# Kernel optimization log

Hardware: AMD Instinct MI355X
Metric: run time of the kernel (lower is better)

Reference implementation:

```python
import jax, jax.numpy as jnp
import numpy as np

B, N, DIM, H, DH, K = 4, 2048, 512, 6, 64, 16
KEEP_PROB = 0.9  # 1 - dropout_rate
LOG2PI = float(np.log(2.0 * np.pi))
LOG_PRIOR = float(np.log(1.0 / K))


def setup_inputs() -> dict:
    key = jax.random.key(0)
    ks = jax.random.split(key, 7)
    inputs_q = jax.random.normal(ks[0], (B, N, DIM), dtype=jnp.float32)
    # decoder-style causal mask, shape [B, 1, q_len, kv_len]
    causal = jnp.tril(jnp.ones((N, N), dtype=jnp.float32))
    mask = jnp.broadcast_to(causal[None, None], (B, 1, N, N))
    # dropout keep mask broadcast across the query dim: [B, H, 1, kv_len]
    keep = jax.random.bernoulli(ks[1], KEEP_PROB, (B, H, 1, N)).astype(jnp.float32)
    w_qkv = jax.random.normal(ks[2], (DIM, 3 * H * DH), dtype=jnp.float32) * 0.02
    w_out = jax.random.normal(ks[3], (H * DH, DIM), dtype=jnp.float32) * 0.02
    mu_lookup = jax.random.normal(ks[4], (K, DIM), dtype=jnp.float32)
    logvar_lookup = jax.random.normal(ks[5], (K, DIM), dtype=jnp.float32) * 0.1
    return {
        "inputs_q": inputs_q,
        "mask": mask,
        "keep": keep,
        "w_qkv": w_qkv,
        "w_out": w_out,
        "mu_lookup": mu_lookup,
        "logvar_lookup": logvar_lookup,
    }


def reference(inputs_q, mask, keep, w_qkv, w_out, mu_lookup, logvar_lookup):
    # --- MultiHeadDotProductAttention (self-attn path) ---
    qkv = (inputs_q @ w_qkv).reshape(B, N, 3, H, DH)  # [B,N,3,H,DH]
    q, k, v = qkv[:, :, 0], qkv[:, :, 1], qkv[:, :, 2]
    # bias: 0 where mask > 0, -1e10 elsewhere (note: no 1/sqrt(d) scaling, as in source)
    bias = jnp.where(mask > 0, 0.0, -1e10)
    attn_weights = jnp.einsum('bqhd,bkhd->bhqk', q, k) + bias  # [B,H,N,N]
    attn_weights = jax.nn.softmax(attn_weights, axis=-1)
    # broadcast dropout: mask shared across the query dim
    attn_weights = attn_weights * keep / KEEP_PROB
    attn_out = jnp.einsum('bhqk,bkhd->bqhd', attn_weights, v)
    attn_out = attn_out.reshape(B, N, H * DH) @ w_out  # [B,N,DIM]

    # --- GMM posterior approx q(y|x) ~= p(y|z) (approx_qy_x, vectorized over k) ---
    z = attn_out.mean(axis=1)  # pooled latent, [B,DIM]
    diff = z[:, None, :] - mu_lookup[None]  # [B,K,DIM]
    llh = -0.5 * jnp.sum(
        diff * diff / jnp.exp(logvar_lookup)[None] + logvar_lookup[None] + LOG2PI,
        axis=-1,
    )  # [B,K]
    logLogit_qy_x = llh + LOG_PRIOR
    qy_x = jax.nn.softmax(logLogit_qy_x, axis=1)  # [B,K]

    # combine mixture mean back in so both branches are live in one output
    return attn_out + (qy_x @ mu_lookup)[:, None, :]
```

## Files before the change

kernel.cpp:

```cpp
#include <hip/hip_runtime.h>
#include <cstdint>
#include <cstddef>

#define NH 6
#define NSEQ 2048
#define DIMD 512
#define BATCH 4
#define HD 384
#define LOG2PI_F 1.8378770664093453f

typedef __attribute__((ext_vector_type(8))) short short8;
typedef __attribute__((ext_vector_type(8))) unsigned short ushort8;
typedef __attribute__((ext_vector_type(4))) unsigned short ushort4v;
typedef __attribute__((ext_vector_type(4))) float floatx4;

__device__ inline unsigned short f2bf(float f){
  unsigned int u = __float_as_uint(f);
  u += 0x7FFFu + ((u>>16)&1u);
  return (unsigned short)(u>>16);
}

#define GLD16(gp, lp) __builtin_amdgcn_global_load_lds( \
  (const __attribute__((address_space(1))) void*)(gp), \
  (__attribute__((address_space(3))) void*)(lp), 16, 0, 0)

__global__ __launch_bounds__(256) void convert_x(
    const float* __restrict__ xq, unsigned short* __restrict__ xbf)
{
  int i = blockIdx.x*256 + threadIdx.x;
  floatx4 v = *(const floatx4*)(xq + (size_t)i*4);
  ushort4v r;
  #pragma unroll
  for(int j=0;j<4;j++) r[j] = f2bf(v[j]);
  *(ushort4v*)(xbf + (size_t)i*4) = r;
}

__global__ __launch_bounds__(256) void wtrans(
    const float* __restrict__ src, unsigned short* __restrict__ dst, int R, int C)
{
  __shared__ __attribute__((aligned(16))) unsigned short Ls[64*72];
  const int t = threadIdx.x;
  const int r = t>>2, c0 = (t&3)*16;
  const int d0 = blockIdx.y*64, n0 = blockIdx.x*64;
  #pragma unroll
  for (int j=0;j<16;j+=4){
    floatx4 v = *(const floatx4*)(src + (size_t)(d0+r)*C + n0 + c0 + j);
    #pragma unroll
    for(int jj=0;jj<4;jj++) Ls[r*72 + c0+j+jj] = f2bf(v[jj]);
  }
  __syncthreads();
  #pragma unroll
  for (int j=0;j<16;j+=8){
    ushort8 o;
    #pragma unroll
    for(int jj=0;jj<8;jj++) o[jj] = Ls[(c0+j+jj)*72 + r];
    *(ushort8*)(dst + (size_t)(n0+r)*R + d0 + c0 + j) = o;
  }
}

__global__ __launch_bounds__(256) void gemm_qkv(
    const unsigned short* __restrict__ A,
    const unsigned short* __restrict__ Bt,
    const float* __restrict__ keep,
    unsigned short* __restrict__ Qo, unsigned short* __restrict__ Ko, unsigned short* __restrict__ Vt)
{
  __shared__ __attribute__((aligned(16))) unsigned short As[128*64];
  __shared__ __attribute__((aligned(16))) unsigned short Bs[128*64];
  const int tid = threadIdx.x;
  const int w = tid>>6, lane = tid&63;
  const int wr = w>>1, wc = w&1;
  const int quad = lane>>4, l16 = lane&15;
  const int tM = blockIdx.y*128, tN = blockIdx.x*128;
  const int r8 = lane>>3, c8 = (lane&7)*8;
  floatx4 acc[4][4];
  floatx4 zed = {0.f,0.f,0.f,0.f};
  #pragma unroll
  for (int i=0;i<4;i++)
    #pragma unroll
    for(int j=0;j<4;j++) acc[i][j] = zed;

  for (int k0=0; k0<512; k0+=64){
    #pragma unroll
    for (int i=0;i<4;i++){
      int row = w*32 + i*8;
      GLD16(A  + (size_t)(tM+row+r8)*512 + k0 + c8, As + row*64);
      GLD16(Bt + (size_t)(tN+row+r8)*512 + k0 + c8, Bs + row*64);
    }
    __syncthreads();
    #pragma unroll
    for (int kk=0; kk<64; kk+=32){
      short8 af[4], bf[4];
      #pragma unroll
      for(int mt=0;mt<4;mt++)
        af[mt] = *(const short8*)(As + (wr*64+mt*16+l16)*64 + kk + quad*8);
      #pragma unroll
      for(int nt=0;nt<4;nt++)
        bf[nt] = *(const short8*)(Bs + (wc*64+nt*16+l16)*64 + kk + quad*8);
      #pragma unroll
      for(int mt=0;mt<4;mt++)
        #pragma unroll
        for(int nt=0;nt<4;nt++)
          acc[mt][nt] = __builtin_amdgcn_mfma_f32_16x16x32_bf16(af[mt], bf[nt], acc[mt][nt], 0,0,0);
    }
    __syncthreads();
  }
  #pragma unroll
  for(int nt=0;nt<4;nt++){
    int gcol = tN + wc*64 + nt*16 + l16;
    int t = gcol/384;
    int rem = gcol - t*384;
    int h = rem>>6, dh = rem&63;
    #pragma unroll
    for(int mt=0;mt<4;mt++){
      int grow = tM + wr*64 + mt*16 + quad*4;
      #pragma unroll
      for(int r=0;r<4;r++){
        int row = grow + r;
        int b = row>>11, n = row & 2047;
        if (t==0)      Qo[(size_t)((b*NH + h)*NSEQ + n)*64 + dh] = f2bf(acc[mt][nt][r]);
        else if (t==1) Ko[(size_t)((b*NH + h)*NSEQ + n)*64 + dh] = f2bf(acc[mt][nt][r]);
        else {
          float kp = keep[(size_t)(b*NH + h)*NSEQ + n];
          Vt[(size_t)((b*NH + h)*64 + dh)*NSEQ + n] = f2bf(acc[mt][nt][r]*kp);
        }
      }
    }
  }
}

__global__ __launch_bounds__(256,3) void attn_kernel(
    const unsigned short* __restrict__ Qg, const unsigned short* __restrict__ Kg,
    const unsigned short* __restrict__ VtG,
    unsigned short* __restrict__ atp)
{
  __shared__ __attribute__((aligned(16))) unsigned short Ks[64*64];
  __shared__ __attribute__((aligned(16))) unsigned short Vs[64*64];
  __shared__ __attribute__((aligned(16))) unsigned short Ps[4*32*72];
  const int tid = threadIdx.x;
  const int w = tid>>6, lane = tid&63;
  const int quad = lane>>4, l16 = lane&15;
  const int bx = 15 - (int)blockIdx.x;
  const int bh = blockIdx.y;
  const int b = bh/NH, h = bh - b*NH;
  const unsigned short* Qb = Qg  + (size_t)bh*NSEQ*64;
  const unsigned short* Kb = Kg  + (size_t)bh*NSEQ*64;
  const unsigned short* Vb = VtG + (size_t)bh*64*NSEQ;
  const int q0 = bx*128 + w*32;
  const int nkt_w  = 2*bx + 1 + (w>>1);
  const int nkt_max= 2*bx + 2;
  const int gr = lane>>3, gc = (lane&7)*8;

  short8 qf[2][2];
  #pragma unroll
  for(int mt=0;mt<2;mt++)
    #pragma unroll
    for(int kc=0;kc<2;kc++)
      qf[mt][kc] = *(const short8*)(Qb + (size_t)(q0+mt*16+l16)*64 + kc*32 + quad*8);

  short8 onesf;
  #pragma unroll
  for(int j=0;j<8;j++) onesf[j] = (short)0x3F80;

  floatx4 O[2][4];
  floatx4 accl[2];
  floatx4 zed = {0.f,0.f,0.f,0.f};
  #pragma unroll
  for(int mt=0;mt<2;mt++){
    #pragma unroll
    for(int dt=0;dt<4;dt++) O[mt][dt] = zed;
    accl[mt] = zed;
  }
  unsigned short* Pw = Ps + w*2304;

  for (int kt=0; kt<nkt_max; kt++){
    const int kB = kt*64;
    #pragma unroll
    for(int ro=0; ro<2; ro++){
      int r0 = ro*32 + w*8;
      GLD16(Kb + (size_t)(kB + r0 + gr)*64 + gc, Ks + r0*64);
      GLD16(Vb + (size_t)(r0 + gr)*NSEQ + kB + gc, Vs + r0*64);
    }
    __syncthreads();
    if (kt < nkt_w){
      short8 kf[4][2];
      #pragma unroll
      for(int nt=0;nt<4;nt++)
        #pragma unroll
        for(int kc=0;kc<2;kc++)
          kf[nt][kc] = *(const short8*)(Ks + (nt*16+l16)*64 + kc*32 + quad*8);

      floatx4 sacc[2][4];
      floatx4 m12 = {-12.f,-12.f,-12.f,-12.f};
      #pragma unroll
      for(int mt=0;mt<2;mt++)
        #pragma unroll
        for(int nt=0;nt<4;nt++) sacc[mt][nt] = m12;
      #pragma unroll
      for(int mt=0;mt<2;mt++)
        #pragma unroll
        for(int nt=0;nt<4;nt++)
          #pragma unroll
          for(int kc=0;kc<2;kc++)
            sacc[mt][nt] = __builtin_amdgcn_mfma_f32_16x16x32_bf16(qf[mt][kc], kf[nt][kc], sacc[mt][nt], 0,0,0);

      const bool dia = (kt == nkt_w-1);
      #pragma unroll
      for(int mt=0;mt<2;mt++){
        #pragma unroll
        for(int nt=0;nt<4;nt++){
          int key = kB + nt*16 + l16;
          #pragma unroll
          for(int r=0;r<4;r++){
            float p = __expf(sacc[mt][nt][r]);
            if (dia) p = (key <= q0 + mt*16 + quad*4 + r) ? p : 0.f;
            Pw[(mt*16+quad*4+r)*72 + nt*16 + l16] = f2bf(p);
          }
        }
      }
      short8 vf[2][4];
      #pragma unroll
      for(int kh=0;kh<2;kh++)
        #pragma unroll
        for(int dt=0;dt<4;dt++)
          vf[kh][dt] = *(const short8*)(Vs + (dt*16+l16)*64 + kh*32 + quad*8);
      #pragma unroll
      for(int kh=0;kh<2;kh++){
        #pragma unroll
        for(int mt=0;mt<2;mt++){
          short8 pf = *(const short8*)(Pw + (mt*16+l16)*72 + kh*32 + quad*8);
          accl[mt] = __builtin_amdgcn_mfma_f32_16x16x32_bf16(pf, onesf, accl[mt], 0,0,0);
          #pragma unroll
          for(int dt=0;dt<4;dt++)
            O[mt][dt] = __builtin_amdgcn_mfma_f32_16x16x32_bf16(pf, vf[kh][dt], O[mt][dt], 0,0,0);
        }
      }
    }
    __syncthreads();
  }

  #pragma unroll
  for(int mt=0;mt<2;mt++){
    #pragma unroll
    for(int r=0;r<4;r++){
      int q = q0 + mt*16 + quad*4 + r;
      float sc = (1.0f/0.9f) / accl[mt][r];
      #pragma unroll
      for(int dt=0;dt<4;dt++)
        atp[((size_t)(b*NSEQ + q))*HD + h*64 + dt*16 + l16] = f2bf(O[mt][dt][r]*sc);
    }
  }
}

__global__ __launch_bounds__(256) void gemm_proj(
    const unsigned short* __restrict__ A,
    const unsigned short* __restrict__ Bt,
    float* __restrict__ Co,
    float* __restrict__ z)
{
  __shared__ __attribute__((aligned(16))) unsigned short As[128*64];
  __shared__ __attribute__((aligned(16))) unsigned short Bs[128*64];
  const int tid = threadIdx.x;
  const int w = tid>>6, lane = tid&63;
  const int wr = w>>1, wc = w&1;
  const int quad = lane>>4, l16 = lane&15;
  const int tM = blockIdx.y*128, tN = blockIdx.x*128;
  const int r8 = lane>>3, c8 = (lane&7)*8;
  floatx4 acc[4][4];
  floatx4 zed = {0.f,0.f,0.f,0.f};
  #pragma unroll
  for (int i=0;i<4;i++)
    #pragma unroll
    for(int j=0;j<4;j++) acc[i][j] = zed;

  for (int k0=0; k0<384; k0+=64){
    #pragma unroll
    for (int i=0;i<4;i++){
      int row = w*32 + i*8;
      GLD16(A  + (size_t)(tM+row+r8)*384 + k0 + c8, As + row*64);
      GLD16(Bt + (size_t)(tN+row+r8)*384 + k0 + c8, Bs + row*64);
    }
    __syncthreads();
    #pragma unroll
    for (int kk=0; kk<64; kk+=32){
      short8 af[4], bf[4];
      #pragma unroll
      for(int mt=0;mt<4;mt++)
        af[mt] = *(const short8*)(As + (wr*64+mt*16+l16)*64 + kk + quad*8);
      #pragma unroll
      for(int nt=0;nt<4;nt++)
        bf[nt] = *(const short8*)(Bs + (wc*64+nt*16+l16)*64 + kk + quad*8);
      #pragma unroll
      for(int mt=0;mt<4;mt++)
        #pragma unroll
        for(int nt=0;nt<4;nt++)
          acc[mt][nt] = __builtin_amdgcn_mfma_f32_16x16x32_bf16(af[mt], bf[nt], acc[mt][nt], 0,0,0);
    }
    __syncthreads();
  }
  #pragma unroll
  for(int mt=0;mt<4;mt++){
    int grow = tM + wr*64 + mt*16 + quad*4;
    #pragma unroll
    for(int nt=0;nt<4;nt++){
      int gcol = tN + wc*64 + nt*16 + l16;
      #pragma unroll
      for(int r=0;r<4;r++)
        Co[(size_t)(grow+r)*512 + gcol] = acc[mt][nt][r];
    }
  }
  #pragma unroll
  for(int nt=0;nt<4;nt++){
    float s = 0.f;
    #pragma unroll
    for(int mt=0;mt<4;mt++)
      #pragma unroll
      for(int r=0;r<4;r++) s += acc[mt][nt][r];
    s += __shfl_xor(s, 16, 64);
    s += __shfl_xor(s, 32, 64);
    if (quad == 0){
      int gcol = tN + wc*64 + nt*16 + l16;
      atomicAdd(&z[(tM>>11)*DIMD + gcol], s);
    }
  }
}

__global__ __launch_bounds__(256) void gmm_kernel(
    const float* __restrict__ z, const float* __restrict__ mu,
    const float* __restrict__ lv, float* __restrict__ c)
{
  __shared__ float sh[16];
  __shared__ float qy[16];
  int tid = threadIdx.x;
  int k = tid>>4, li = tid&15;
  int b = blockIdx.x;
  float part = 0.f;
  for(int d=li; d<DIMD; d+=16){
    float zz = z[b*DIMD+d] * (1.0f/2048.0f);
    float m = mu[k*DIMD+d], l = lv[k*DIMD+d];
    float diff = zz - m;
    part += diff*diff*__expf(-l) + l + LOG2PI_F;
  }
  #pragma unroll
  for(int off=8;off>=1;off>>=1) part += __shfl_xor(part, off, 64);
  if (li==0) sh[k] = part;
  __syncthreads();
  if (tid<16){
    float logit = -0.5f*sh[tid];
    float mx = logit;
    #pragma unroll
    for(int off=8;off>=1;off>>=1) mx = fmaxf(mx, __shfl_xor(mx, off, 64));
    float e = __expf(logit-mx);
    float se = e;
    #pragma unroll
    for(int off=8;off>=1;off>>=1) se += __shfl_xor(se, off, 64);
    qy[tid] = e/se;
  }
  __syncthreads();
  for(int d=tid; d<DIMD; d+=256){
    float accv = 0.f;
    #pragma unroll
    for(int kk=0;kk<16;kk++) accv += qy[kk]*mu[kk*DIMD+d];
    c[b*DIMD+d] = accv;
  }
}

__global__ __launch_bounds__(256) void final_add(
    const float* __restrict__ ao, const float* __restrict__ c, float* __restrict__ out)
{
  size_t i = ((size_t)blockIdx.x*256 + threadIdx.x)*4;
  int d = (int)(i & 511);
  int b = (int)(i >> 20);
  floatx4 a = *(const floatx4*)(ao + i);
  floatx4 cc = *(const floatx4*)(c + b*DIMD + d);
  *(floatx4*)(out + i) = a + cc;
}

extern "C" void kernel_launch(void* const* d_in, const int* in_sizes, int n_in,
                              void* d_out, int out_size, void* d_ws, size_t ws_size,
                              hipStream_t stream) {
  const float* inputs_q = (const float*)d_in[0];
  const float* keep  = (const float*)d_in[2];
  const float* w_qkv = (const float*)d_in[3];
  const float* w_out = (const float*)d_in[4];
  const float* mu    = (const float*)d_in[5];
  const float* lv    = (const float*)d_in[6];
  float* out = (float*)d_out;
  char* ws = (char*)d_ws;
  size_t off = 0;
  auto alloc = [&](size_t bytes){ void* p = ws + off; off += (bytes + 255) & ~(size_t)255; return p; };
  unsigned short* Qb  = (unsigned short*)alloc((size_t)24*2048*64*2);
  unsigned short* Kb  = (unsigned short*)alloc((size_t)24*2048*64*2);
  unsigned short* Vt  = (unsigned short*)alloc((size_t)24*64*2048*2);
  unsigned short* xbf = (unsigned short*)alloc((size_t)8192*512*2);
  unsigned short* wqT = (unsigned short*)alloc((size_t)1152*512*2);
  unsigned short* woT = (unsigned short*)alloc((size_t)512*384*2);
  unsigned short* atp = (unsigned short*)alloc((size_t)8192*384*2);
  float* ao = (float*)alloc((size_t)8192*512*4);
  float* z  = (float*)alloc((size_t)4*512*4);
  float* c  = (float*)alloc((size_t)4*512*4);

  hipMemsetAsync(z, 0, 4*512*4, stream);
  convert_x<<<4096, 256, 0, stream>>>(inputs_q, xbf);
  wtrans<<<dim3(18,8), 256, 0, stream>>>(w_qkv, wqT, 512, 1152);
  wtrans<<<dim3(8,6),  256, 0, stream>>>(w_out, woT, 384, 512);
  gemm_qkv<<<dim3(9,64), 256, 0, stream>>>(xbf, wqT, keep, Qb, Kb, Vt);
  attn_kernel<<<dim3(16,24), 256, 0, stream>>>(Qb, Kb, Vt, atp);
  gemm_proj<<<dim3(4,64), 256, 0, stream>>>(atp, woT, ao, z);
  gmm_kernel<<<4, 256, 0, stream>>>(z, mu, lv, c);
  final_add<<<4096, 256, 0, stream>>>(ao, c, out);
}
```

Baseline: 265.8 us.

## Restructure QKV epilogue, add V transpose, split attention into single-wave blocks

The QKV GEMM now stages results in shared memory and writes coalesced 16-byte rows, zeroing dropped V rows instead of scaling them. A separate kernel transposes V. Attention is rewritten as 1536 single-wave blocks, one per 32-query chunk, ordered heaviest first. These read K and V directly from global memory into registers with double-buffered K loads, dropping the shared-memory staging and barriers. Projection output goes straight to the final buffer with a swapped grid order, at the cost of an extra kernel and more uncached global reads in attention.

Measured after the change: 246.3 us. -7.3%, faster.

```diff
diff --git a/kernel.cpp b/kernel.cpp
--- a/kernel.cpp
+++ b/kernel.cpp
@@ -58,11 +58,232 @@
   }
 }
 
+__global__ __launch_bounds__(256) void vtrans(
+    const unsigned short* __restrict__ Vo, unsigned short* __restrict__ Vt)
+{
+  __shared__ __attribute__((aligned(16))) unsigned short Ls[64*72];
+  const int t = threadIdx.x;
+  const int r = t>>2, c0 = (t&3)*16;
+  const int n0 = blockIdx.x*64, bh = blockIdx.y;
+  #pragma unroll
+  for (int j=0;j<16;j+=8)
+    *(ushort8*)(Ls + r*72 + c0 + j) = *(const ushort8*)(Vo + ((size_t)bh*NSEQ + n0 + r)*64 + c0 + j);
+  __syncthreads();
+  #pragma unroll
+  for (int j=0;j<16;j+=8){
+    ushort8 o;
+    #pragma unroll
+    for(int jj=0;jj<8;jj++) o[jj] = Ls[(c0+j+jj)*72 + r];
+    *(ushort8*)(Vt + ((size_t)bh*64 + r)*NSEQ + n0 + c0 + j) = o;
+  }
+}
+
 __global__ __launch_bounds__(256) void gemm_qkv(
     const unsigned short* __restrict__ A,
     const unsigned short* __restrict__ Bt,
     const float* __restrict__ keep,
-    unsigned short* __restrict__ Qo, unsigned short* __restrict__ Ko, unsigned short* __restrict__ Vt)
+    unsigned short* __restrict__ Qo, unsigned short* __restrict__ Ko, unsigned short* __restrict__ Vo)
+{
+  __shared__ __attribute__((aligned(16))) unsigned short Cs[128*132];
+  unsigned short* As = Cs;
+  unsigned short* Bs = Cs + 128*64;
+  const int tid = threadIdx.x;
+  const int w = tid>>6, lane = tid&63;
+  const int wr = w>>1, wc = w&1;
+  const int quad = lane>>4, l16 = lane&15;
+  const int tM = blockIdx.x*128, tN = blockIdx.y*128;
+  const int r8 = lane>>3, c8 = (lane&7)*8;
+  floatx4 acc[4][4];
+  floatx4 zed = {0.f,0.f,0.f,0.f};
+  #pragma unroll
+  for (int i=0;i<4;i++)
+    #pragma unroll
+    for(int j=0;j<4;j++) acc[i][j] = zed;
+
+  for (int k0=0; k0<512; k0+=64){
+    #pragma unroll
+    for (int i=0;i<4;i++){
+      int row = w*32 + i*8;
+      GLD16(A  + (size_t)(tM+row+r8)*512 + k0 + c8, As + row*64);
+      GLD16(Bt + (size_t)(tN+row+r8)*512 + k0 + c8, Bs + row*64);
+    }
+    __syncthreads();
+    #pragma unroll
+    for (int kk=0; kk<64; kk+=32){
+      short8 af[4], bf[4];
+      #pragma unroll
+      for(int mt=0;mt<4;mt++)
+        af[mt] = *(const short8*)(As + (wr*64+mt*16+l16)*64 + kk + quad*8);
+      #pragma unroll
+      for(int nt=0;nt<4;nt++)
+        bf[nt] = *(const short8*)(Bs + (wc*64+nt*16+l16)*64 + kk + quad*8);
+      #pragma unroll
+      for(int mt=0;mt<4;mt++)
+        #pragma unroll
+        for(int nt=0;nt<4;nt++)
+          acc[mt][nt] = __builtin_amdgcn_mfma_f32_16x16x32_bf16(af[mt], bf[nt], acc[mt][nt], 0,0,0);
+    }
+    __syncthreads();
+  }
+  #pragma unroll
+  for(int mt=0;mt<4;mt++)
+    #pragma unroll
+    for(int nt=0;nt<4;nt++)
+      #pragma unroll
+      for(int r=0;r<4;r++)
+        Cs[(wr*64+mt*16+quad*4+r)*132 + wc*64+nt*16+l16] = f2bf(acc[mt][nt][r]);
+  __syncthreads();
+  const int row = tid>>1, colh = (tid&1)*64;
+  const int gcol0 = tN + colh;
+  const int t = gcol0/384, rem = gcol0 - t*384, h = rem>>6;
+  const int grow = tM + row, b = grow>>11, n = grow & 2047;
+  unsigned short* dst = (t==0 ? Qo : (t==1 ? Ko : Vo)) + ((size_t)((b*NH+h)*NSEQ+n))*64;
+  bool vzero = false;
+  if (t==2) vzero = (keep[(size_t)(b*NH+h)*NSEQ+n] < 0.5f);
+  ushort8 zz;
+  #pragma unroll
+  for(int q2=0;q2<8;q2++) zz[q2]=0;
+  #pragma unroll
+  for(int j=0;j<8;j++){
+    ushort8 v = *(const ushort8*)(Cs + row*132 + colh + j*8);
+    *(ushort8*)(dst + j*8) = vzero ? zz : v;
+  }
+}
+
+__global__ __launch_bounds__(64) void attn_kernel(
+    const unsigned short* __restrict__ Qg, const unsigned short* __restrict__ Kg,
+    const unsigned short* __restrict__ VtG,
+    unsigned short* __restrict__ atp)
+{
+  __shared__ __attribute__((aligned(16))) unsigned short Ps[32*72];
+  const int lane = threadIdx.x;
+  const int quad = lane>>4, l16 = lane&15;
+  const int bid = blockIdx.x;
+  const int idx = bid>>3;
+  const int bh  = (bid&7) + 8*(idx % 3);
+  const int c   = 63 - idx/3;
+  const int b = bh/NH, h = bh - b*NH;
+  const unsigned short* Qb = Qg  + (size_t)bh*NSEQ*64;
+  const unsigned short* Kb = Kg  + (size_t)bh*NSEQ*64;
+  const unsigned short* Vb = VtG + (size_t)bh*64*NSEQ;
+  const int q0 = c*32;
+  const int nkt = (c>>1) + 1;
+
+  short8 qf[2][2];
+  #pragma unroll
+  for(int mt=0;mt<2;mt++)
+    #pragma unroll
+    for(int kc=0;kc<2;kc++)
+      qf[mt][kc] = *(const short8*)(Qb + (size_t)(q0+mt*16+l16)*64 + kc*32 + quad*8);
+
+  short8 onesf;
+  #pragma unroll
+  for(int j=0;j<8;j++) onesf[j] = (short)0x3F80;
+
+  floatx4 O[2][4];
+  floatx4 accl[2];
+  floatx4 zed = {0.f,0.f,0.f,0.f};
+  #pragma unroll
+  for(int mt=0;mt<2;mt++){
+    #pragma unroll
+    for(int dt=0;dt<4;dt++) O[mt][dt] = zed;
+    accl[mt] = zed;
+  }
+
+  short8 kA[4][2], kB2[4][2];
+  auto loadK = [&](int kt, short8 (&kf)[4][2]){
+    const unsigned short* kp0 = Kb + (size_t)kt*64*64;
+    #pragma unroll
+    for(int nt=0;nt<4;nt++)
+      #pragma unroll
+      for(int kc=0;kc<2;kc++)
+        kf[nt][kc] = *(const short8*)(kp0 + (size_t)(nt*16+l16)*64 + kc*32 + quad*8);
+  };
+
+  auto tile = [&](int kt, short8 (&kf)[4][2]){
+    const int kB = kt*64;
+    short8 vf[2][4];
+    const unsigned short* vp0 = Vb + kB;
+    #pragma unroll
+    for(int kh=0;kh<2;kh++)
+      #pragma unroll
+      for(int dt=0;dt<4;dt++)
+        vf[kh][dt] = *(const short8*)(vp0 + (size_t)(dt*16+l16)*NSEQ + kh*32 + quad*8);
+
+    floatx4 sacc[2][4];
+    floatx4 m12 = {-12.f,-12.f,-12.f,-12.f};
+    #pragma unroll
+    for(int mt=0;mt<2;mt++)
+      #pragma unroll
+      for(int nt=0;nt<4;nt++) sacc[mt][nt] = m12;
+    #pragma unroll
+    for(int mt=0;mt<2;mt++)
+      #pragma unroll
+      for(int nt=0;nt<4;nt++)
+        #pragma unroll
+        for(int kc=0;kc<2;kc++)
+          sacc[mt][nt] = __builtin_amdgcn_mfma_f32_16x16x32_bf16(qf[mt][kc], kf[nt][kc], sacc[mt][nt], 0,0,0);
+
+    const bool dia = (kt == nkt-1);
+    #pragma unroll
+    for(int mt=0;mt<2;mt++){
+      #pragma unroll
+      for(int nt=0;nt<4;nt++){
+        int key = kB + nt*16 + l16;
+        #pragma unroll
+        for(int r=0;r<4;r++){
+          float p = __expf(sacc[mt][nt][r]);
+          if (dia) p = (key <= q0 + mt*16 + quad*4 + r) ? p : 0.f;
+          Ps[(mt*16+quad*4+r)*72 + nt*16 + l16] = f2bf(p);
+        }
+      }
+    }
+    #pragma unroll
+    for(int kh=0;kh<2;kh++){
+      #pragma unroll
+      for(int mt=0;mt<2;mt++){
+        short8 pf = *(const short8*)(Ps + (mt*16+l16)*72 + kh*32 + quad*8);
+        accl[mt] = __builtin_amdgcn_mfma_f32_16x16x32_bf16(pf, onesf, accl[mt], 0,0,0);
+        #pragma unroll
+        for(int dt=0;dt<4;dt++)
+          O[mt][dt] = __builtin_amdgcn_mfma_f32_16x16x32_bf16(pf, vf[kh][dt], O[mt][dt], 0,0,0);
+      }
+    }
+  };
+
+  loadK(0, kA);
+  int kt = 0;
+  while (true){
+    loadK(kt+1 < nkt ? kt+1 : kt, kB2);
+    tile(kt, kA);
+    kt++; if (kt >= nkt) break;
+    loadK(kt+1 < nkt ? kt+1 : kt, kA);
+    tile(kt, kB2);
+    kt++; if (kt >= nkt) break;
+  }
+
+  #pragma unroll
+  for(int mt=0;mt<2;mt++)
+    #pragma unroll
+    for(int r=0;r<4;r++){
+      float sc2 = (1.0f/0.9f) / accl[mt][r];
+      #pragma unroll
+      for(int dt=0;dt<4;dt++)
+        Ps[(mt*16+quad*4+r)*72 + dt*16 + l16] = f2bf(O[mt][dt][r]*sc2);
+    }
+  const int orow = lane>>1, ohalf = (lane&1)*32;
+  const int q = q0 + orow;
+  unsigned short* dstp = atp + ((size_t)(b*NSEQ+q))*HD + h*64 + ohalf;
+  #pragma unroll
+  for(int j=0;j<4;j++)
+    *(ushort8*)(dstp + j*8) = *(const ushort8*)(Ps + orow*72 + ohalf + j*8);
+}
+
+__global__ __launch_bounds__(256) void gemm_proj(
+    const unsigned short* __restrict__ A,
+    const unsigned short* __restrict__ Bt,
+    float* __restrict__ out,
+    float* __restrict__ z)
 {
   __shared__ __attribute__((aligned(16))) unsigned short As[128*64];
   __shared__ __attribute__((aligned(16))) unsigned short Bs[128*64];
@@ -70,7 +291,7 @@
   const int w = tid>>6, lane = tid&63;
   const int wr = w>>1, wc = w&1;
   const int quad = lane>>4, l16 = lane&15;
-  const int tM = blockIdx.y*128, tN = blockIdx.x*128;
+  const int tM = blockIdx.x*128, tN = blockIdx.y*128;
   const int r8 = lane>>3, c8 = (lane&7)*8;
   floatx4 acc[4][4];
   floatx4 zed = {0.f,0.f,0.f,0.f};
@@ -79,12 +300,12 @@
     #pragma unroll
     for(int j=0;j<4;j++) acc[i][j] = zed;
 
-  for (int k0=0; k0<512; k0+=64){
+  for (int k0=0; k0<384; k0+=64){
     #pragma unroll
     for (int i=0;i<4;i++){
       int row = w*32 + i*8;
-      GLD16(A  + (size_t)(tM+row+r8)*512 + k0 + c8, As + row*64);
-      GLD16(Bt + (size_t)(tN+row+r8)*512 + k0 + c8, Bs + row*64);
+      GLD16(A  + (size_t)(tM+row+r8)*384 + k0 + c8, As + row*64);
+      GLD16(Bt + (size_t)(tN+row+r8)*384 + k0 + c8, Bs + row*64);
     }
     __syncthreads();
     #pragma unroll
@@ -105,199 +326,6 @@
     __syncthreads();
   }
   #pragma unroll
-  for(int nt=0;nt<4;nt++){
-    int gcol = tN + wc*64 + nt*16 + l16;
-    int t = gcol/384;
-    int rem = gcol - t*384;
-    int h = rem>>6, dh = rem&63;
-    #pragma unroll
-    for(int mt=0;mt<4;mt++){
-      int grow = tM + wr*64 + mt*16 + quad*4;
-      #pragma unroll
-      for(int r=0;r<4;r++){
-        int row = grow + r;
-        int b = row>>11, n = row & 2047;
-        if (t==0)      Qo[(size_t)((b*NH + h)*NSEQ + n)*64 + dh] = f2bf(acc[mt][nt][r]);
-        else if (t==1) Ko[(size_t)((b*NH + h)*NSEQ + n)*64 + dh] = f2bf(acc[mt][nt][r]);
-        else {
-          float kp = keep[(size_t)(b*NH + h)*NSEQ + n];
-          Vt[(size_t)((b*NH + h)*64 + dh)*NSEQ + n] = f2bf(acc[mt][nt][r]*kp);
-        }
-      }
-    }
-  }
-}
-
-__global__ __launch_bounds__(256,3) void attn_kernel(
-    const unsigned short* __restrict__ Qg, const unsigned short* __restrict__ Kg,
-    const unsigned short* __restrict__ VtG,
-    unsigned short* __restrict__ atp)
-{
-  __shared__ __attribute__((aligned(16))) unsigned short Ks[64*64];
-  __shared__ __attribute__((aligned(16))) unsigned short Vs[64*64];
-  __shared__ __attribute__((aligned(16))) unsigned short Ps[4*32*72];
-  const int tid = threadIdx.x;
-  const int w = tid>>6, lane = tid&63;
-  const int quad = lane>>4, l16 = lane&15;
-  const int bx = 15 - (int)blockIdx.x;
-  const int bh = blockIdx.y;
-  const int b = bh/NH, h = bh - b*NH;
-  const unsigned short* Qb = Qg  + (size_t)bh*NSEQ*64;
-  const unsigned short* Kb = Kg  + (size_t)bh*NSEQ*64;
-  const unsigned short* Vb = VtG + (size_t)bh*64*NSEQ;
-  const int q0 = bx*128 + w*32;
-  const int nkt_w  = 2*bx + 1 + (w>>1);
-  const int nkt_max= 2*bx + 2;
-  const int gr = lane>>3, gc = (lane&7)*8;
-
-  short8 qf[2][2];
-  #pragma unroll
-  for(int mt=0;mt<2;mt++)
-    #pragma unroll
-    for(int kc=0;kc<2;kc++)
-      qf[mt][kc] = *(const short8*)(Qb + (size_t)(q0+mt*16+l16)*64 + kc*32 + quad*8);
-
-  short8 onesf;
-  #pragma unroll
-  for(int j=0;j<8;j++) onesf[j] = (short)0x3F80;
-
-  floatx4 O[2][4];
-  floatx4 accl[2];
-  floatx4 zed = {0.f,0.f,0.f,0.f};
-  #pragma unroll
-  for(int mt=0;mt<2;mt++){
-    #pragma unroll
-    for(int dt=0;dt<4;dt++) O[mt][dt] = zed;
-    accl[mt] = zed;
-  }
-  unsigned short* Pw = Ps + w*2304;
-
-  for (int kt=0; kt<nkt_max; kt++){
-    const int kB = kt*64;
-    #pragma unroll
-    for(int ro=0; ro<2; ro++){
-      int r0 = ro*32 + w*8;
-      GLD16(Kb + (size_t)(kB + r0 + gr)*64 + gc, Ks + r0*64);
-      GLD16(Vb + (size_t)(r0 + gr)*NSEQ + kB + gc, Vs + r0*64);
-    }
-    __syncthreads();
-    if (kt < nkt_w){
-      short8 kf[4][2];
-      #pragma unroll
-      for(int nt=0;nt<4;nt++)
-        #pragma unroll
-        for(int kc=0;kc<2;kc++)
-          kf[nt][kc] = *(const short8*)(Ks + (nt*16+l16)*64 + kc*32 + quad*8);
-
-      floatx4 sacc[2][4];
-      floatx4 m12 = {-12.f,-12.f,-12.f,-12.f};
-      #pragma unroll
-      for(int mt=0;mt<2;mt++)
-        #pragma unroll
-        for(int nt=0;nt<4;nt++) sacc[mt][nt] = m12;
-      #pragma unroll
-      for(int mt=0;mt<2;mt++)
-        #pragma unroll
-        for(int nt=0;nt<4;nt++)
-          #pragma unroll
-          for(int kc=0;kc<2;kc++)
-            sacc[mt][nt] = __builtin_amdgcn_mfma_f32_16x16x32_bf16(qf[mt][kc], kf[nt][kc], sacc[mt][nt], 0,0,0);
-
-      const bool dia = (kt == nkt_w-1);
-      #pragma unroll
-      for(int mt=0;mt<2;mt++){
-        #pragma unroll
-        for(int nt=0;nt<4;nt++){
-          int key = kB + nt*16 + l16;
-          #pragma unroll
-          for(int r=0;r<4;r++){
-            float p = __expf(sacc[mt][nt][r]);
-            if (dia) p = (key <= q0 + mt*16 + quad*4 + r) ? p : 0.f;
-            Pw[(mt*16+quad*4+r)*72 + nt*16 + l16] = f2bf(p);
-          }
-        }
-      }
-      short8 vf[2][4];
-      #pragma unroll
-      for(int kh=0;kh<2;kh++)
-        #pragma unroll
-        for(int dt=0;dt<4;dt++)
-          vf[kh][dt] = *(const short8*)(Vs + (dt*16+l16)*64 + kh*32 + quad*8);
-      #pragma unroll
-      for(int kh=0;kh<2;kh++){
-        #pragma unroll
-        for(int mt=0;mt<2;mt++){
-          short8 pf = *(const short8*)(Pw + (mt*16+l16)*72 + kh*32 + quad*8);
-          accl[mt] = __builtin_amdgcn_mfma_f32_16x16x32_bf16(pf, onesf, accl[mt], 0,0,0);
-          #pragma unroll
-          for(int dt=0;dt<4;dt++)
-            O[mt][dt] = __builtin_amdgcn_mfma_f32_16x16x32_bf16(pf, vf[kh][dt], O[mt][dt], 0,0,0);
-        }
-      }
-    }
-    __syncthreads();
-  }
-
-  #pragma unroll
-  for(int mt=0;mt<2;mt++){
-    #pragma unroll
-    for(int r=0;r<4;r++){
-      int q = q0 + mt*16 + quad*4 + r;
-      float sc = (1.0f/0.9f) / accl[mt][r];
-      #pragma unroll
-      for(int dt=0;dt<4;dt++)
-        atp[((size_t)(b*NSEQ + q))*HD + h*64 + dt*16 + l16] = f2bf(O[mt][dt][r]*sc);
-    }
-  }
-}
-
-__global__ __launch_bounds__(256) void gemm_proj(
-    const unsigned short* __restrict__ A,
-    const unsigned short* __restrict__ Bt,
-    float* __restrict__ Co,
-    float* __restrict__ z)
-{
-  __shared__ __attribute__((aligned(16))) unsigned short As[128*64];
-  __shared__ __attribute__((aligned(16))) unsigned short Bs[128*64];
-  const int tid = threadIdx.x;
-  const int w = tid>>6, lane = tid&63;
-  const int wr = w>>1, wc = w&1;
-  const int quad = lane>>4, l16 = lane&15;
-  const int tM = blockIdx.y*128, tN = blockIdx.x*128;
-  const int r8 = lane>>3, c8 = (lane&7)*8;
-  floatx4 acc[4][4];
-  floatx4 zed = {0.f,0.f,0.f,0.f};
-  #pragma unroll
-  for (int i=0;i<4;i++)
-    #pragma unroll
-    for(int j=0;j<4;j++) acc[i][j] = zed;
-
-  for (int k0=0; k0<384; k0+=64){
-    #pragma unroll
-    for (int i=0;i<4;i++){
-      int row = w*32 + i*8;
-      GLD16(A  + (size_t)(tM+row+r8)*384 + k0 + c8, As + row*64);
-      GLD16(Bt + (size_t)(tN+row+r8)*384 + k0 + c8, Bs + row*64);
-    }
-    __syncthreads();
-    #pragma unroll
-    for (int kk=0; kk<64; kk+=32){
-      short8 af[4], bf[4];
-      #pragma unroll
-      for(int mt=0;mt<4;mt++)
-        af[mt] = *(const short8*)(As + (wr*64+mt*16+l16)*64 + kk + quad*8);
-      #pragma unroll
-      for(int nt=0;nt<4;nt++)
-        bf[nt] = *(const short8*)(Bs + (wc*64+nt*16+l16)*64 + kk + quad*8);
-      #pragma unroll
-      for(int mt=0;mt<4;mt++)
-        #pragma unroll
-        for(int nt=0;nt<4;nt++)
-          acc[mt][nt] = __builtin_amdgcn_mfma_f32_16x16x32_bf16(af[mt], bf[nt], acc[mt][nt], 0,0,0);
-    }
-    __syncthreads();
-  }
-  #pragma unroll
   for(int mt=0;mt<4;mt++){
     int grow = tM + wr*64 + mt*16 + quad*4;
     #pragma unroll
@@ -305,7 +333,7 @@
       int gcol = tN + wc*64 + nt*16 + l16;
       #pragma unroll
       for(int r=0;r<4;r++)
-        Co[(size_t)(grow+r)*512 + gcol] = acc[mt][nt][r];
+        out[(size_t)(grow+r)*512 + gcol] = acc[mt][nt][r];
     }
   }
   #pragma unroll
@@ -365,12 +393,12 @@
 }
 
 __global__ __launch_bounds__(256) void final_add(
-    const float* __restrict__ ao, const float* __restrict__ c, float* __restrict__ out)
+    float* __restrict__ out, const float* __restrict__ c)
 {
   size_t i = ((size_t)blockIdx.x*256 + threadIdx.x)*4;
   int d = (int)(i & 511);
   int b = (int)(i >> 20);
-  floatx4 a = *(const floatx4*)(ao + i);
+  floatx4 a = *(const floatx4*)(out + i);
   floatx4 cc = *(const floatx4*)(c + b*DIMD + d);
   *(floatx4*)(out + i) = a + cc;
 }
@@ -390,12 +418,12 @@
   auto alloc = [&](size_t bytes){ void* p = ws + off; off += (bytes + 255) & ~(size_t)255; return p; };
   unsigned short* Qb  = (unsigned short*)alloc((size_t)24*2048*64*2);
   unsigned short* Kb  = (unsigned short*)alloc((size_t)24*2048*64*2);
+  unsigned short* Vo  = (unsigned short*)alloc((size_t)24*2048*64*2);
   unsigned short* Vt  = (unsigned short*)alloc((size_t)24*64*2048*2);
   unsigned short* xbf = (unsigned short*)alloc((size_t)8192*512*2);
   unsigned short* wqT = (unsigned short*)alloc((size_t)1152*512*2);
   unsigned short* woT = (unsigned short*)alloc((size_t)512*384*2);
   unsigned short* atp = (unsigned short*)alloc((size_t)8192*384*2);
-  float* ao = (float*)alloc((size_t)8192*512*4);
   float* z  = (float*)alloc((size_t)4*512*4);
   float* c  = (float*)alloc((size_t)4*512*4);
 
@@ -403,9 +431,10 @@
   convert_x<<<4096, 256, 0, stream>>>(inputs_q, xbf);
   wtrans<<<dim3(18,8), 256, 0, stream>>>(w_qkv, wqT, 512, 1152);
   wtrans<<<dim3(8,6),  256, 0, stream>>>(w_out, woT, 384, 512);
-  gemm_qkv<<<dim3(9,64), 256, 0, stream>>>(xbf, wqT, keep, Qb, Kb, Vt);
-  attn_kernel<<<dim3(16,24), 256, 0, stream>>>(Qb, Kb, Vt, atp);
-  gemm_proj<<<dim3(4,64), 256, 0, stream>>>(atp, woT, ao, z);
+  gemm_qkv<<<dim3(64,9), 256, 0, stream>>>(xbf, wqT, keep, Qb, Kb, Vo);
+  vtrans<<<dim3(32,24), 256, 0, stream>>>(Vo, Vt);
+  attn_kernel<<<1536, 64, 0, stream>>>(Qb, Kb, Vt, atp);
+  gemm_proj<<<dim3(64,4), 256, 0, stream>>>(atp, woT, out, z);
   gmm_kernel<<<4, 256, 0, stream>>>(z, mu, lv, c);
-  final_add<<<4096, 256, 0, stream>>>(ao, c, out);
-}
+  final_add<<<4096, 256, 0, stream>>>(out, c);
+}
```
